# Performance work log

Measured on AMD Instinct MI355X. Metric: run time of the kernel, lower is better.

The kernel has to match this reference:

```python
import jax, jax.numpy as jnp
import numpy as np

B, T, D, H = 8, 2048, 1024, 64


def setup_inputs() -> dict:
    key = jax.random.key(0)
    k1, k2, k3, k4 = jax.random.split(key, 4)
    scale = 1.0 / np.sqrt(D)
    return {
        "x": jax.random.normal(k1, (B, T, D), dtype=jnp.float32),
        "Wq": jax.random.normal(k2, (D, H), dtype=jnp.float32) * scale,
        "Wk": jax.random.normal(k3, (D, H), dtype=jnp.float32) * scale,
        "Wv": jax.random.normal(k4, (D, H), dtype=jnp.float32) * scale,
    }


def reference(x, Wq, Wk, Wv):
    # x: [B, T, D]; projections to [B, T, H]
    q = jnp.einsum("btd,dh->bth", x, Wq)
    k = jnp.einsum("btd,dh->bth", x, Wk)
    v = jnp.einsum("btd,dh->bth", x, Wv)
    head_size = k.shape[-1]
    # scores: [B, T, T], scaled by head_size**-0.5
    wei = jnp.einsum("bqh,bkh->bqk", q, k) * (head_size ** -0.5)
    t = q.shape[1]
    causal = jnp.tril(jnp.ones((t, t), dtype=bool))  # [T, T]
    wei = jnp.where(causal, wei, -jnp.inf)
    wei = jax.nn.softmax(wei, axis=-1)
    # dropout p=0.0 (eval) -> identity
    out = jnp.einsum("bqk,bkh->bqh", wei, v)  # [B, T, H]
    return out
```

## Files before the change

### kernel.cpp

```cpp
#include <hip/hip_runtime.h>
#include <hip/hip_bf16.h>

typedef __attribute__((ext_vector_type(8))) __bf16 bf16x8;
typedef __attribute__((ext_vector_type(4))) float f32x4;

namespace {
constexpr int kB = 8;
constexpr int kT = 2048;
constexpr int kD = 1024;
constexpr int kH = 64;
}

__global__ __launch_bounds__(256) void wt_kernel(
    const float* __restrict__ Wq, const float* __restrict__ Wk,
    const float* __restrict__ Wv, __bf16* __restrict__ wtf) {
  const int wid = threadIdx.x >> 6;
  const int lane = threadIdx.x & 63;
  const int lr = lane & 15;
  const int lg = lane >> 4;
  const int p = blockIdx.x * 4 + wid;
  const int nt = p >> 5;
  const int ks = p & 31;
  const float* W = (nt < 4) ? Wq : ((nt < 8) ? Wk : Wv);
  const float scale = (nt < 4) ? 0.18033688011112042f : 1.0f;
  const int col = (nt & 3) * 16 + lr;
  bf16x8 v;
#pragma unroll
  for (int j = 0; j < 8; ++j)
    v[j] = (__bf16)(W[(size_t)(ks * 32 + lg * 8 + j) * kH + col] * scale);
  *(bf16x8*)(wtf + (size_t)p * 512 + lane * 8) = v;
}

__global__ __launch_bounds__(256, 2) void proj_kernel(
    const float* __restrict__ x, const __bf16* __restrict__ wtf,
    __bf16* __restrict__ Q, __bf16* __restrict__ kf, __bf16* __restrict__ vf) {
  __shared__ alignas(16) char lds_raw[65536];
  float* p_s = (float*)lds_raw;

  const int tid = threadIdx.x;
  const int wid = tid >> 6;
  const int lane = tid & 63;
  const int lr = lane & 15;
  const int lg = lane >> 4;
  const int row0 = blockIdx.x * 32;

#pragma unroll
  for (int i = 0; i < 16; ++i) {
    const int c = i * 256 + tid;
    const int row = c >> 7;
    const int kc = c & 127;
    const float* src = x + (size_t)(row0 + row) * kD + kc * 8;
    const float4 a = ((const float4*)src)[0];
    const float4 b = ((const float4*)src)[1];
    bf16x8 v;
    v[0] = (__bf16)a.x; v[1] = (__bf16)a.y; v[2] = (__bf16)a.z; v[3] = (__bf16)a.w;
    v[4] = (__bf16)b.x; v[5] = (__bf16)b.y; v[6] = (__bf16)b.z; v[7] = (__bf16)b.w;
    const int byte = row * 2048 + ((kc * 16) ^ ((row & 7) << 4));
    *(bf16x8*)(lds_raw + byte) = v;
  }
  __syncthreads();

  f32x4 acc[2][12];
#pragma unroll
  for (int a = 0; a < 2; ++a)
#pragma unroll
    for (int nt = 0; nt < 12; ++nt) acc[a][nt] = (f32x4)(0.0f);

  const int swz = (lr & 7) << 4;
#pragma unroll 2
  for (int i = 0; i < 8; ++i) {
    const int kb = (wid * 256 + i * 32 + lg * 8) * 2;
    const bf16x8 a0 = *(const bf16x8*)(lds_raw + lr * 2048 + (kb ^ swz));
    const bf16x8 a1 = *(const bf16x8*)(lds_raw + 32768 + lr * 2048 + (kb ^ swz));
#pragma unroll
    for (int nt = 0; nt < 12; ++nt) {
      const bf16x8 bfrag =
          *(const bf16x8*)(wtf + (size_t)(nt * 32 + wid * 8 + i) * 512 + lane * 8);
      acc[0][nt] = __builtin_amdgcn_mfma_f32_16x16x32_bf16(a0, bfrag, acc[0][nt], 0, 0, 0);
      acc[1][nt] = __builtin_amdgcn_mfma_f32_16x16x32_bf16(a1, bfrag, acc[1][nt], 0, 0, 0);
    }
  }

  const int col = tid & 15;
  const int rowq = tid >> 4;
#pragma unroll
  for (int p = 0; p < 2; ++p) {
    __syncthreads();
#pragma unroll
    for (int j = 0; j < 12; ++j)
      *(f32x4*)&p_s[((wid * 12 + j) * 64 + lane) * 4] = acc[p][j];
    __syncthreads();
    const size_t g = (size_t)row0 + p * 16 + rowq;
    const int b = (int)(g >> 11);
    const int t = (int)(g & 2047);
#pragma unroll
    for (int j = 0; j < 12; ++j) {
      const int base = ((j * 64 + (rowq >> 2) * 16 + col) << 2) | (rowq & 3);
      const float v =
          p_s[base] + p_s[base + 3072] + p_s[base + 6144] + p_s[base + 9216];
      if (j < 4) {
        Q[g * kH + j * 16 + col] = (__bf16)v;
      } else if (j < 8) {
        const int h = (j - 4) * 16 + col;
        const int r = t & 31;
        const int lrk = ((r >> 3) << 2) | (r & 3);
        const int sub = (r >> 2) & 1;
        const int dh = h >> 5;
        const int lgk = (h & 31) >> 3;
        const int jj = h & 7;
        kf[(((size_t)b * 64 + (t >> 5)) * 4 + sub * 2 + dh) * 512 +
           (lgk * 16 + lrk) * 8 + jj] = (__bf16)v;
      } else {
        vf[(((size_t)b * 64 + (t >> 5)) * 4 + (j - 8)) * 512 +
           ((t & 31) >> 3) * 128 + col * 8 + (t & 7)] = (__bf16)v;
      }
    }
  }
}

__global__ __launch_bounds__(256, 4) void attn_kernel(
    const __bf16* __restrict__ Q, const __bf16* __restrict__ kf,
    const __bf16* __restrict__ vf, float* __restrict__ out) {
  __shared__ alignas(16) float o_s[4][16][68];
  __shared__ float m_s[4][16], l_s[4][4][16];

  const int wid = threadIdx.x >> 6;
  const int lane = threadIdx.x & 63;
  const int lr = lane & 15;
  const int lg = lane >> 4;
  const int b = blockIdx.y;
  const int qt = (int)gridDim.x - 1 - (int)blockIdx.x;
  const int q0 = qt * 16;

  const __bf16* Qb = Q + (size_t)b * kT * kH;
  const __bf16* Kf = kf + (size_t)b * 131072 + lane * 8;
  const __bf16* Vf = vf + (size_t)b * 131072 + lane * 8;

  const bf16x8 aq0 = *(const bf16x8*)(Qb + (size_t)(q0 + lr) * kH + lg * 8);
  const bf16x8 aq1 = *(const bf16x8*)(Qb + (size_t)(q0 + lr) * kH + 32 + lg * 8);

  f32x4 o[4];
#pragma unroll
  for (int i = 0; i < 4; ++i) o[i] = (f32x4)(0.0f);
  float m = -1e30f, l = 0.0f;

  const int ntiles = (q0 + 16 + 31) >> 5;

  bf16x8 ka[4], va[4];
  {
    const int t0c = (wid < ntiles) ? wid : 0;
#pragma unroll
    for (int c = 0; c < 4; ++c) {
      ka[c] = *(const bf16x8*)(Kf + ((size_t)t0c * 4 + c) * 512);
      va[c] = *(const bf16x8*)(Vf + ((size_t)t0c * 4 + c) * 512);
    }
  }

  for (int t = wid; t < ntiles; t += 4) {
    const int tn = (t + 4 < ntiles) ? (t + 4) : t;
    bf16x8 kn[4], vn[4];
#pragma unroll
    for (int c = 0; c < 4; ++c) {
      kn[c] = *(const bf16x8*)(Kf + ((size_t)tn * 4 + c) * 512);
      vn[c] = *(const bf16x8*)(Vf + ((size_t)tn * 4 + c) * 512);
    }

    const int kv = t * 32;
    f32x4 s0 = (f32x4)(0.0f), s1 = (f32x4)(0.0f);
    s0 = __builtin_amdgcn_mfma_f32_16x16x32_bf16(ka[0], aq0, s0, 0, 0, 0);
    s0 = __builtin_amdgcn_mfma_f32_16x16x32_bf16(ka[1], aq1, s0, 0, 0, 0);
    s1 = __builtin_amdgcn_mfma_f32_16x16x32_bf16(ka[2], aq0, s1, 0, 0, 0);
    s1 = __builtin_amdgcn_mfma_f32_16x16x32_bf16(ka[3], aq1, s1, 0, 0, 0);

    if (kv + 31 > q0) {
      const int q = q0 + lr;
#pragma unroll
      for (int r = 0; r < 4; ++r) {
        if (kv + 8 * lg + r > q) s0[r] = -1e30f;
        if (kv + 8 * lg + 4 + r > q) s1[r] = -1e30f;
      }
    }

    const float pm = fmaxf(fmaxf(fmaxf(s0[0], s0[1]), fmaxf(s0[2], s0[3])),
                           fmaxf(fmaxf(s1[0], s1[1]), fmaxf(s1[2], s1[3])));
    if (!__all(pm - m <= 8.0f)) {
      float t2 = fmaxf(pm, __shfl_xor(pm, 16, 64));
      t2 = fmaxf(t2, __shfl_xor(t2, 32, 64));
      const float mn = fmaxf(m, t2);
      const float alpha = exp2f(m - mn);
#pragma unroll
      for (int ht = 0; ht < 4; ++ht) o[ht] = o[ht] * alpha;
      l *= alpha;
      m = mn;
    }

    float sum = 0.0f;
    bf16x8 pb;
#pragma unroll
    for (int r = 0; r < 4; ++r) {
      const float p0 = exp2f(s0[r] - m);
      const float p1 = exp2f(s1[r] - m);
      sum += p0 + p1;
      pb[r] = (__bf16)p0;
      pb[r + 4] = (__bf16)p1;
    }
    l += sum;

#pragma unroll
    for (int ht = 0; ht < 4; ++ht)
      o[ht] = __builtin_amdgcn_mfma_f32_16x16x32_bf16(va[ht], pb, o[ht], 0, 0, 0);

#pragma unroll
    for (int c = 0; c < 4; ++c) {
      ka[c] = kn[c];
      va[c] = vn[c];
    }
  }

#pragma unroll
  for (int ht = 0; ht < 4; ++ht)
    *(f32x4*)&o_s[wid][lr][ht * 16 + lg * 4] = o[ht];
  if (lg == 0) m_s[wid][lr] = m;
  l_s[wid][lg][lr] = l;
  __syncthreads();

  const int ti = threadIdx.x;
  const int q = ti & 15;
  const int hb = ti >> 4;
  float mm = fmaxf(fmaxf(m_s[0][q], m_s[1][q]), fmaxf(m_s[2][q], m_s[3][q]));
  f32x4 acc = (f32x4)(0.0f);
  float ll = 0.0f;
#pragma unroll
  for (int w = 0; w < 4; ++w) {
    const float sc = exp2f(m_s[w][q] - mm);
    const float lw =
        l_s[w][0][q] + l_s[w][1][q] + l_s[w][2][q] + l_s[w][3][q];
    ll += sc * lw;
    const f32x4 ov = *(const f32x4*)&o_s[w][q][hb * 4];
    acc += ov * sc;
  }
  const float inv = 1.0f / ll;
  *(f32x4*)(out + ((size_t)b * kT + q0 + q) * kH + hb * 4) = acc * inv;
}

extern "C" void kernel_launch(void* const* d_in, const int* in_sizes, int n_in,
                              void* d_out, int out_size, void* d_ws, size_t ws_size,
                              hipStream_t stream) {
  (void)in_sizes; (void)n_in; (void)out_size; (void)ws_size;
  const float* x  = (const float*)d_in[0];
  const float* Wq = (const float*)d_in[1];
  const float* Wk = (const float*)d_in[2];
  const float* Wv = (const float*)d_in[3];
  float* out = (float*)d_out;

  char* ws = (char*)d_ws;
  __bf16* wtf = (__bf16*)(ws);
  __bf16* Qp  = (__bf16*)(ws + 393216);
  __bf16* kfp = (__bf16*)(ws + 393216 + 2097152);
  __bf16* vfp = (__bf16*)(ws + 393216 + 2 * 2097152);

  wt_kernel<<<96, 256, 0, stream>>>(Wq, Wk, Wv, wtf);
  proj_kernel<<<kB * kT / 32, 256, 0, stream>>>(x, wtf, Qp, kfp, vfp);
  attn_kernel<<<dim3(kT / 16, kB), 256, 0, stream>>>(Qp, kfp, vfp, out);
}
```

Measured before the change: 134.3 us.

## Stage x per-wave in LDS without barrier and coalesce projection output stores

Each wave now loads and converts only the 256-column K-slice of x it will consume into its own LDS region, so the block-wide barrier before the MFMA loop is dropped. Projection results for Q, K and V are written into an LDS staging area in their final packed layouts and then copied out with one 16-byte vector store per thread per tensor, replacing scattered 2-byte global stores. This targets uncoalesced global writes and barrier stalls, at the cost of extra LDS traffic and a barrier at the end.

```diff
diff --git a/kernel.cpp b/kernel.cpp
--- a/kernel.cpp
+++ b/kernel.cpp
@@ -36,6 +36,7 @@
     __bf16* __restrict__ Q, __bf16* __restrict__ kf, __bf16* __restrict__ vf) {
   __shared__ alignas(16) char lds_raw[65536];
   float* p_s = (float*)lds_raw;
+  char* ostage = lds_raw + 49152;
 
   const int tid = threadIdx.x;
   const int wid = tid >> 6;
@@ -44,21 +45,24 @@
   const int lg = lane >> 4;
   const int row0 = blockIdx.x * 32;
 
-#pragma unroll
-  for (int i = 0; i < 16; ++i) {
-    const int c = i * 256 + tid;
-    const int row = c >> 7;
-    const int kc = c & 127;
-    const float* src = x + (size_t)(row0 + row) * kD + kc * 8;
-    const float4 a = ((const float4*)src)[0];
-    const float4 b = ((const float4*)src)[1];
-    bf16x8 v;
-    v[0] = (__bf16)a.x; v[1] = (__bf16)a.y; v[2] = (__bf16)a.z; v[3] = (__bf16)a.w;
-    v[4] = (__bf16)b.x; v[5] = (__bf16)b.y; v[6] = (__bf16)b.z; v[7] = (__bf16)b.w;
-    const int byte = row * 2048 + ((kc * 16) ^ ((row & 7) << 4));
-    *(bf16x8*)(lds_raw + byte) = v;
-  }
-  __syncthreads();
+  char* wstage = lds_raw + wid * 16384;
+  {
+    const int srow = lane >> 5;
+    const int scol = (lane & 31) * 8;
+    const float* xq = x + (size_t)row0 * kD + wid * 256;
+#pragma unroll
+    for (int i = 0; i < 16; ++i) {
+      const int row = i * 2 + srow;
+      const float* src = xq + (size_t)row * kD + scol;
+      const float4 a = ((const float4*)src)[0];
+      const float4 b = ((const float4*)src)[1];
+      bf16x8 v;
+      v[0] = (__bf16)a.x; v[1] = (__bf16)a.y; v[2] = (__bf16)a.z; v[3] = (__bf16)a.w;
+      v[4] = (__bf16)b.x; v[5] = (__bf16)b.y; v[6] = (__bf16)b.z; v[7] = (__bf16)b.w;
+      const int byte = row * 512 + ((scol * 2) ^ ((row & 7) << 4));
+      *(bf16x8*)(wstage + byte) = v;
+    }
+  }
 
   f32x4 acc[2][12];
 #pragma unroll
@@ -69,9 +73,9 @@
   const int swz = (lr & 7) << 4;
 #pragma unroll 2
   for (int i = 0; i < 8; ++i) {
-    const int kb = (wid * 256 + i * 32 + lg * 8) * 2;
-    const bf16x8 a0 = *(const bf16x8*)(lds_raw + lr * 2048 + (kb ^ swz));
-    const bf16x8 a1 = *(const bf16x8*)(lds_raw + 32768 + lr * 2048 + (kb ^ swz));
+    const int kb = lg * 16 + i * 64;
+    const bf16x8 a0 = *(const bf16x8*)(wstage + lr * 512 + (kb ^ swz));
+    const bf16x8 a1 = *(const bf16x8*)(wstage + (16 + lr) * 512 + (kb ^ swz));
 #pragma unroll
     for (int nt = 0; nt < 12; ++nt) {
       const bf16x8 bfrag =
@@ -90,32 +94,38 @@
     for (int j = 0; j < 12; ++j)
       *(f32x4*)&p_s[((wid * 12 + j) * 64 + lane) * 4] = acc[p][j];
     __syncthreads();
-    const size_t g = (size_t)row0 + p * 16 + rowq;
-    const int b = (int)(g >> 11);
-    const int t = (int)(g & 2047);
+    const int tl = p * 16 + rowq;
 #pragma unroll
     for (int j = 0; j < 12; ++j) {
       const int base = ((j * 64 + (rowq >> 2) * 16 + col) << 2) | (rowq & 3);
       const float v =
           p_s[base] + p_s[base + 3072] + p_s[base + 6144] + p_s[base + 9216];
       if (j < 4) {
-        Q[g * kH + j * 16 + col] = (__bf16)v;
+        ((__bf16*)ostage)[tl * 64 + j * 16 + col] = (__bf16)v;
       } else if (j < 8) {
         const int h = (j - 4) * 16 + col;
-        const int r = t & 31;
-        const int lrk = ((r >> 3) << 2) | (r & 3);
-        const int sub = (r >> 2) & 1;
+        const int lrk = ((tl >> 3) << 2) | (tl & 3);
+        const int sub = (tl >> 2) & 1;
         const int dh = h >> 5;
         const int lgk = (h & 31) >> 3;
         const int jj = h & 7;
-        kf[(((size_t)b * 64 + (t >> 5)) * 4 + sub * 2 + dh) * 512 +
-           (lgk * 16 + lrk) * 8 + jj] = (__bf16)v;
+        ((__bf16*)(ostage + 4096))[(sub * 2 + dh) * 512 + (lgk * 16 + lrk) * 8 + jj] =
+            (__bf16)v;
       } else {
-        vf[(((size_t)b * 64 + (t >> 5)) * 4 + (j - 8)) * 512 +
-           ((t & 31) >> 3) * 128 + col * 8 + (t & 7)] = (__bf16)v;
+        ((__bf16*)(ostage + 8192))[(j - 8) * 512 + (tl >> 3) * 128 + col * 8 +
+                                   (tl & 7)] = (__bf16)v;
       }
     }
   }
+  __syncthreads();
+
+  const int b = row0 >> 11;
+  const int tc = (row0 & 2047) >> 5;
+  const size_t cbase = ((size_t)b * 64 + tc) * 2048;
+  *(bf16x8*)(Q + (size_t)row0 * kH + tid * 8) =
+      *(const bf16x8*)(ostage + tid * 16);
+  *(bf16x8*)(kf + cbase + tid * 8) = *(const bf16x8*)(ostage + 4096 + tid * 16);
+  *(bf16x8*)(vf + cbase + tid * 8) = *(const bf16x8*)(ostage + 8192 + tid * 16);
 }
 
 __global__ __launch_bounds__(256, 4) void attn_kernel(
```

After: 134.5 us. About the same (+0.2%).
